# Performance work log

Measured on AMD Instinct MI355X. Metric: run time of the kernel, lower is better.

## Reference

```python
import jax, jax.numpy as jnp
import numpy as np

N = 100000
E = 1600000
F_IN = 128
NHID = 50
NOUT = 50


def gcn_conv(x, W, b, src, dst, n):
    # x: [N, Fin] -> transform first (PyG GCNConv order)
    h = x @ W  # [N, Fout]
    # symmetric normalization with self-loops already included in src/dst
    ones = jnp.ones(src.shape[0], dtype=h.dtype)
    deg = jax.ops.segment_sum(ones, dst, num_segments=n)  # in-degree incl self-loop
    dinv = jnp.where(deg > 0, jax.lax.rsqrt(deg), 0.0)
    norm = dinv[src] * dinv[dst]  # [E']
    msgs = h[src] * norm[:, None]  # gather + scale, [E', Fout]
    out = jax.ops.segment_sum(msgs, dst, num_segments=n)  # scatter-add
    return out + b


def setup_inputs() -> dict:
    key = jax.random.key(0)
    k1, k2, k3, k4, k5, k6 = jax.random.split(key, 6)
    x = jax.random.normal(k1, (N, F_IN), dtype=jnp.float32)
    edge_index = jax.random.randint(k2, (2, E), 0, N, dtype=jnp.int64) if jax.config.read('jax_enable_x64') else jax.random.randint(k2, (2, E), 0, N, dtype=jnp.int32)
    # Glorot-ish init for weights
    W1 = jax.random.normal(k3, (F_IN, NHID), dtype=jnp.float32) * (1.0 / np.sqrt(F_IN))
    b1 = jnp.zeros((NHID,), dtype=jnp.float32)
    W2 = jax.random.normal(k4, (NHID, NOUT), dtype=jnp.float32) * (1.0 / np.sqrt(NHID))
    b2 = jnp.zeros((NOUT,), dtype=jnp.float32)
    return {"x": x, "W1": W1, "b1": b1, "W2": W2, "b2": b2, "edge_index": edge_index}


def reference(x, W1, b1, W2, b2, edge_index):
    n = x.shape[0]
    # add self-loops once (shared by both layers)
    loop = jnp.arange(n, dtype=edge_index.dtype)
    src = jnp.concatenate([edge_index[0], loop])
    dst = jnp.concatenate([edge_index[1], loop])
    h = gcn_conv(x, W1, b1, src, dst, n)
    h = jax.nn.relu(h)
    # dropout is identity in eval mode (training=False)
    out = gcn_conv(h, W2, b2, src, dst, n)
    return out
```

## Files before the change

kernel.cpp:

```cpp
#include <hip/hip_runtime.h>
#include <hip/hip_fp16.h>

#define FIN 128
#define FH 50
#define HSTRIDE 64
#define MAXNB 1024
#define BSHIFT 7
#define BSIZE 128
#define CAP 3072
#define PCHUNK 2048
#define SRCMASK 0x01FFFFFFu

typedef _Float16 f16x8 __attribute__((ext_vector_type(8)));
typedef float f32x4 __attribute__((ext_vector_type(4)));


__global__ __launch_bounds__(256) void partition_kernel(const int* __restrict__ src,
                                                        const int* __restrict__ dst,
                                                        int* __restrict__ gcursor,
                                                        unsigned int* __restrict__ packed,
                                                        int E, int NB) {
    __shared__ int hist[MAXNB];
    __shared__ int wbase[MAXNB];
    int t = threadIdx.x;
    int base = blockIdx.x * PCHUNK;
    for (int i = t; i < NB; i += 256) hist[i] = 0;
    __syncthreads();
#pragma unroll
    for (int i = 0; i < PCHUNK / 256; i++) {
        int e = base + t + i * 256;
        if (e < E) atomicAdd(&hist[dst[e] >> BSHIFT], 1);
    }
    __syncthreads();
    for (int i = t; i < NB; i += 256) {
        int c = hist[i];
        wbase[i] = c ? atomicAdd(&gcursor[i], c) : 0;
        hist[i] = 0;
    }
    __syncthreads();
#pragma unroll
    for (int i = 0; i < PCHUNK / 256; i++) {
        int e = base + t + i * 256;
        if (e < E) {
            unsigned int s = (unsigned int)src[e];
            int d = dst[e];
            int b = d >> BSHIFT;
            int off = atomicAdd(&hist[b], 1);
            packed[(size_t)b * CAP + wbase[b] + off] =
                ((unsigned int)(d & (BSIZE - 1)) << 25) | s;
        }
    }
}

__global__ __launch_bounds__(256) void bucket_build_kernel(const unsigned int* __restrict__ packed,
                                                           const int* __restrict__ gcursor,
                                                           int* __restrict__ rbeg,
                                                           int* __restrict__ rend,
                                                           float* __restrict__ dinv,
                                                           int* __restrict__ csr, int n) {
    __shared__ int degl[BSIZE];
    __shared__ int excl[BSIZE];
    __shared__ int lcur[BSIZE];
    int b = blockIdx.x;
    int t = threadIdx.x;
    int nbeg = b << BSHIFT;
    int sbase = b * CAP;
    int cnt = gcursor[b];
    if (t < BSIZE) degl[t] = 0;
    __syncthreads();
    for (int e = t; e < cnt; e += 256)
        atomicAdd(&degl[packed[sbase + e] >> 25], 1);
    __syncthreads();
    int v = (t < BSIZE) ? degl[t] : 0;
    if (t < BSIZE) excl[t] = v;
    __syncthreads();
    for (int off = 1; off < BSIZE; off <<= 1) {
        int add = (t >= off && t < BSIZE) ? excl[t - off] : 0;
        __syncthreads();
        if (t < BSIZE) excl[t] += add;
        __syncthreads();
    }
    if (t < BSIZE) {
        int ex = excl[t] - v;
        int node = nbeg + t;
        if (node < n) {
            rbeg[node] = sbase + ex;
            rend[node] = sbase + ex + v;
            dinv[node] = rsqrtf((float)v + 1.0f);
        }
        lcur[t] = ex;
    }
    __syncthreads();
    for (int e = t; e < cnt; e += 256) {
        unsigned int w = packed[sbase + e];
        int off = atomicAdd(&lcur[w >> 25], 1);
        csr[sbase + off] = (int)(w & SRCMASK);
    }
}


__global__ __launch_bounds__(256) void wcvt_kernel(const float* __restrict__ W1,
                                                   const float* __restrict__ W2,
                                                   _Float16* __restrict__ WF1,
                                                   _Float16* __restrict__ WF2) {
    int idx = blockIdx.x * 256 + threadIdx.x;
    if (idx < 4 * 4 * 64 * 8) {
        int i = idx & 7, lane = (idx >> 3) & 63, tile = idx >> 9;
        int ct = tile & 3, kt = tile >> 2;
        int k = kt * 32 + ((lane >> 4) << 3) + i;
        int c = ct * 16 + (lane & 15);
        WF1[idx] = (c < FH) ? (_Float16)W1[k * FH + c] : (_Float16)0.f;
    } else if (idx < 8192 + 2 * 4 * 64 * 8) {
        int g = idx - 8192;
        int i = g & 7, lane = (g >> 3) & 63, tile = g >> 9;
        int ct = tile & 3, kt = tile >> 2;
        int k = kt * 32 + ((lane >> 4) << 3) + i;
        int c = ct * 16 + (lane & 15);
        WF2[g] = (k < FH && c < FH) ? (_Float16)W2[k * FH + c] : (_Float16)0.f;
    }
}

__global__ __launch_bounds__(256) void gemm1_kernel(
    const float* __restrict__ x, const _Float16* __restrict__ WF,
    const float* __restrict__ dinv, __half* __restrict__ hs1,
    __half* __restrict__ hs2, int n) {
    int t = threadIdx.x;
    if (blockIdx.x == 0) {
        if (t < HSTRIDE)           hs1[((size_t)n << 6) + t] = __float2half(0.f);
        else if (t < 2 * HSTRIDE)  hs2[((size_t)n << 6) + (t - HSTRIDE)] = __float2half(0.f);
    }
    int tile = blockIdx.x * 4 + (t >> 6);
    int l = t & 63;
    int mt = (n + 15) >> 4;
    if (tile >= mt) return;
    int arow = tile * 16 + (l & 15);
    if (arow >= n) arow = n - 1;
    const f16x8* WB = (const f16x8*)WF;
    f32x4 acc[4] = {{0.f,0.f,0.f,0.f},{0.f,0.f,0.f,0.f},
                    {0.f,0.f,0.f,0.f},{0.f,0.f,0.f,0.f}};
#pragma unroll
    for (int kt = 0; kt < 4; kt++) {
        const float* xp = x + (size_t)arow * FIN + kt * 32 + ((l >> 4) << 3);
        float4 v0 = *(const float4*)xp;
        float4 v1 = *(const float4*)(xp + 4);
        float vs[8] = {v0.x, v0.y, v0.z, v0.w, v1.x, v1.y, v1.z, v1.w};
        f16x8 hi, lo;
#pragma unroll
        for (int i = 0; i < 8; i++) {
            _Float16 h = (_Float16)vs[i];
            hi[i] = h;
            lo[i] = (_Float16)(vs[i] - (float)h);
        }
#pragma unroll
        for (int ct = 0; ct < 4; ct++) {
            f16x8 b = WB[(kt * 4 + ct) * 64 + l];
            acc[ct] = __builtin_amdgcn_mfma_f32_16x16x32_f16(hi, b, acc[ct], 0, 0, 0);
            acc[ct] = __builtin_amdgcn_mfma_f32_16x16x32_f16(lo, b, acc[ct], 0, 0, 0);
        }
    }
    int rbase = tile * 16 + ((l >> 4) << 2);
    float dv[4];
#pragma unroll
    for (int j = 0; j < 4; j++) {
        int r = rbase + j;
        dv[j] = dinv[r < n ? r : 0];
    }
#pragma unroll
    for (int ct = 0; ct < 4; ct++) {
        int col = ct * 16 + (l & 15);
        if (col < FH) {
#pragma unroll
            for (int j = 0; j < 4; j++) {
                int r = rbase + j;
                if (r < n)
                    hs1[((size_t)r << 6) + col] = __float2half(acc[ct][j] * dv[j]);
            }
        }
    }
}

__global__ __launch_bounds__(256) void gemm2_kernel(
    const float* __restrict__ h1, const _Float16* __restrict__ WF,
    const float* __restrict__ dinv, __half* __restrict__ hs2, int n) {
    int t = threadIdx.x;
    int tile = blockIdx.x * 4 + (t >> 6);
    int l = t & 63;
    int mt = (n + 15) >> 4;
    if (tile >= mt) return;
    int arow = tile * 16 + (l & 15);
    if (arow >= n) arow = n - 1;
    const f16x8* WB = (const f16x8*)WF;
    const float* hp = h1 + (size_t)arow * FH;
    f32x4 acc[4] = {{0.f,0.f,0.f,0.f},{0.f,0.f,0.f,0.f},
                    {0.f,0.f,0.f,0.f},{0.f,0.f,0.f,0.f}};
#pragma unroll
    for (int kt = 0; kt < 2; kt++) {
        int k0 = kt * 32 + ((l >> 4) << 3);
        float vs[8];
        if (kt == 0) {
            const float2* p2 = (const float2*)(hp + k0);
#pragma unroll
            for (int q = 0; q < 4; q++) {
                float2 v = p2[q];
                vs[2 * q] = v.x;
                vs[2 * q + 1] = v.y;
            }
        } else {
#pragma unroll
            for (int i = 0; i < 8; i++) {
                int k = k0 + i;
                float v = hp[k < FH ? k : 0];
                vs[i] = (k < FH) ? v : 0.f;
            }
        }
        f16x8 hi, lo;
#pragma unroll
        for (int i = 0; i < 8; i++) {
            _Float16 h = (_Float16)vs[i];
            hi[i] = h;
            lo[i] = (_Float16)(vs[i] - (float)h);
        }
#pragma unroll
        for (int ct = 0; ct < 4; ct++) {
            f16x8 b = WB[(kt * 4 + ct) * 64 + l];
            acc[ct] = __builtin_amdgcn_mfma_f32_16x16x32_f16(hi, b, acc[ct], 0, 0, 0);
            acc[ct] = __builtin_amdgcn_mfma_f32_16x16x32_f16(lo, b, acc[ct], 0, 0, 0);
        }
    }
    int rbase = tile * 16 + ((l >> 4) << 2);
    float dv[4];
#pragma unroll
    for (int j = 0; j < 4; j++) {
        int r = rbase + j;
        dv[j] = dinv[r < n ? r : 0];
    }
#pragma unroll
    for (int ct = 0; ct < 4; ct++) {
        int col = ct * 16 + (l & 15);
        if (col < FH) {
#pragma unroll
            for (int j = 0; j < 4; j++) {
                int r = rbase + j;
                if (r < n)
                    hs2[((size_t)r << 6) + col] = __float2half(acc[ct][j] * dv[j]);
            }
        }
    }
}

__global__ __launch_bounds__(256) void gather_kernel(
    const __half* __restrict__ hs, const int* __restrict__ rbeg,
    const int* __restrict__ rend, const int* __restrict__ csr,
    const float* __restrict__ dinv, const float* __restrict__ b,
    float* __restrict__ out, int n, int do_relu) {
    int wid = blockIdx.x * 4 + (threadIdx.x >> 6);
    int lane = threadIdx.x & 63;
    if (wid >= n) return;
    int sub = lane >> 5;
    int cp  = lane & 31;
    const __half2* h2 = (const __half2*)hs;
    int beg = rbeg[wid];
    int end = rend[wid];
    float2 acc0 = {0.f, 0.f}, acc1 = {0.f, 0.f};
    if (sub == 0) acc0 = __half22float2(h2[(wid << 5) + cp]);
    for (int base = beg; base < end; base += 64) {
        int rem = end - base;
        int idxs = ((lane < rem) ? csr[base + lane] : n) << 5;
        int cnt = rem < 64 ? rem : 64;
        for (int j = 0; j < cnt; j += 16) {
#pragma unroll
            for (int u = 0; u < 8; u += 2) {
                int s0 = __shfl(idxs, j + 2 * u + sub);
                int s1 = __shfl(idxs, j + 2 * (u + 1) + sub);
                float2 f0 = __half22float2(h2[s0 + cp]);
                float2 f1 = __half22float2(h2[s1 + cp]);
                acc0.x += f0.x; acc0.y += f0.y;
                acc1.x += f1.x; acc1.y += f1.y;
            }
        }
    }
    float ax = (acc0.x + acc1.x);
    float ay = (acc0.y + acc1.y);
    ax += __shfl_xor(ax, 32);
    ay += __shfl_xor(ay, 32);
    if (sub == 0 && cp < FH / 2) {
        float dv = dinv[wid];
        const float2* b2 = (const float2*)b;
        float2 bb = b2[cp];
        float ox = fmaf(dv, ax, bb.x);
        float oy = fmaf(dv, ay, bb.y);
        if (do_relu) { ox = fmaxf(ox, 0.f); oy = fmaxf(oy, 0.f); }
        float2* op = (float2*)(out + (size_t)wid * FH);
        op[cp] = make_float2(ox, oy);
    }
}

extern "C" void kernel_launch(void* const* d_in, const int* in_sizes, int n_in,
                              void* d_out, int out_size, void* d_ws, size_t ws_size,
                              hipStream_t stream) {
    const float* x  = (const float*)d_in[0];
    const float* W1 = (const float*)d_in[1];
    const float* b1 = (const float*)d_in[2];
    const float* W2 = (const float*)d_in[3];
    const float* b2 = (const float*)d_in[4];
    const int*   ei = (const int*)d_in[5];

    int n = in_sizes[0] / FIN;
    int E = in_sizes[5] / 2;
    const int* src = ei;
    const int* dst = ei + E;
    int NB = (n + BSIZE - 1) >> BSHIFT;

    char* ws = (char*)d_ws;
    size_t off = 0;
    auto alloc = [&](size_t bytes) {
        void* p = ws + off;
        off = (off + bytes + 511) & ~(size_t)511;
        return p;
    };
    size_t hs_bytes   = (size_t)(n + 1) * HSTRIDE * 2;
    size_t slab_bytes = (size_t)NB * CAP * 4;
    size_t un_bytes   = slab_bytes > hs_bytes ? slab_bytes : hs_bytes;

    int*          gcursor = (int*)alloc((size_t)MAXNB * 4);
    int*          rbeg    = (int*)alloc((size_t)n * 4);
    int*          rend    = (int*)alloc((size_t)n * 4);
    float*        dinv    = (float*)alloc((size_t)n * 4);
    int*          csr     = (int*)alloc(slab_bytes);
    __half*       hs1     = (__half*)alloc(hs_bytes);
    _Float16*     wf1     = (_Float16*)alloc((size_t)8192 * 2);
    _Float16*     wf2     = (_Float16*)alloc((size_t)4096 * 2);
    void*         un      = alloc(un_bytes);
    unsigned int* packed  = (unsigned int*)un;
    __half*       hs2     = (__half*)un;
    float*        out     = (float*)d_out;

    hipMemsetAsync(gcursor, 0, (size_t)MAXNB * 4, stream);

    wcvt_kernel<<<(8192 + 4096 + 255) / 256, 256, 0, stream>>>(W1, W2, wf1, wf2);

    int pChunks = (E + PCHUNK - 1) / PCHUNK;
    partition_kernel<<<pChunks, 256, 0, stream>>>(src, dst, gcursor, packed, E, NB);
    bucket_build_kernel<<<NB, 256, 0, stream>>>(packed, gcursor, rbeg, rend, dinv, csr, n);

    int mt = (n + 15) / 16;
    int gBlocks = (mt + 3) / 4;
    int gatherBlocks = (n + 3) / 4;

    gemm1_kernel<<<gBlocks, 256, 0, stream>>>(x, wf1, dinv, hs1, hs2, n);
    gather_kernel<<<gatherBlocks, 256, 0, stream>>>(hs1, rbeg, rend, csr, dinv, b1, out, n, 1);
    gemm2_kernel<<<gBlocks, 256, 0, stream>>>(out, wf2, dinv, hs2, n);
    gather_kernel<<<gatherBlocks, 256, 0, stream>>>(hs2, rbeg, rend, csr, dinv, b2, out, n, 0);
}
```

Baseline: 251.3 us.

## Replace shared-memory partition histogram with per-edge padded global atomics

```diff
diff --git a/kernel.cpp b/kernel.cpp
--- a/kernel.cpp
+++ b/kernel.cpp
@@ -8,8 +8,9 @@
 #define BSHIFT 7
 #define BSIZE 128
 #define CAP 3072
-#define PCHUNK 2048
+#define EPB 2048
 #define SRCMASK 0x01FFFFFFu
+#define CPAD 16
 
 typedef _Float16 f16x8 __attribute__((ext_vector_type(8)));
 typedef float f32x4 __attribute__((ext_vector_type(4)));
@@ -19,35 +20,30 @@
                                                         const int* __restrict__ dst,
                                                         int* __restrict__ gcursor,
                                                         unsigned int* __restrict__ packed,
-                                                        int E, int NB) {
-    __shared__ int hist[MAXNB];
-    __shared__ int wbase[MAXNB];
-    int t = threadIdx.x;
-    int base = blockIdx.x * PCHUNK;
-    for (int i = t; i < NB; i += 256) hist[i] = 0;
-    __syncthreads();
-#pragma unroll
-    for (int i = 0; i < PCHUNK / 256; i++) {
-        int e = base + t + i * 256;
-        if (e < E) atomicAdd(&hist[dst[e] >> BSHIFT], 1);
-    }
-    __syncthreads();
-    for (int i = t; i < NB; i += 256) {
-        int c = hist[i];
-        wbase[i] = c ? atomicAdd(&gcursor[i], c) : 0;
-        hist[i] = 0;
-    }
-    __syncthreads();
-#pragma unroll
-    for (int i = 0; i < PCHUNK / 256; i++) {
-        int e = base + t + i * 256;
-        if (e < E) {
-            unsigned int s = (unsigned int)src[e];
-            int d = dst[e];
+                                                        int E) {
+    int e0 = (blockIdx.x * 256 + threadIdx.x) * 8;
+    if (e0 >= E) return;
+    if (e0 + 8 <= E) {
+        int4 d0 = *(const int4*)(dst + e0);
+        int4 d1 = *(const int4*)(dst + e0 + 4);
+        int4 s0 = *(const int4*)(src + e0);
+        int4 s1 = *(const int4*)(src + e0 + 4);
+        int ds[8] = {d0.x, d0.y, d0.z, d0.w, d1.x, d1.y, d1.z, d1.w};
+        int ss[8] = {s0.x, s0.y, s0.z, s0.w, s1.x, s1.y, s1.z, s1.w};
+#pragma unroll
+        for (int i = 0; i < 8; i++) {
+            int b = ds[i] >> BSHIFT;
+            int off = atomicAdd(&gcursor[b << 4], 1);
+            packed[(size_t)b * CAP + off] =
+                ((unsigned int)(ds[i] & (BSIZE - 1)) << 25) | (unsigned int)ss[i];
+        }
+    } else {
+        for (int i = 0; i < 8 && e0 + i < E; i++) {
+            int d = dst[e0 + i];
             int b = d >> BSHIFT;
-            int off = atomicAdd(&hist[b], 1);
-            packed[(size_t)b * CAP + wbase[b] + off] =
-                ((unsigned int)(d & (BSIZE - 1)) << 25) | s;
+            int off = atomicAdd(&gcursor[b << 4], 1);
+            packed[(size_t)b * CAP + off] =
+                ((unsigned int)(d & (BSIZE - 1)) << 25) | (unsigned int)src[e0 + i];
         }
     }
 }
@@ -65,11 +61,16 @@
     int t = threadIdx.x;
     int nbeg = b << BSHIFT;
     int sbase = b * CAP;
-    int cnt = gcursor[b];
+    int cnt = gcursor[b << 4];
     if (t < BSIZE) degl[t] = 0;
     __syncthreads();
-    for (int e = t; e < cnt; e += 256)
-        atomicAdd(&degl[packed[sbase + e] >> 25], 1);
+    for (int e4 = t * 4; e4 < cnt; e4 += 1024) {
+        uint4 w = *(const uint4*)(packed + sbase + e4);
+        unsigned int wv[4] = {w.x, w.y, w.z, w.w};
+#pragma unroll
+        for (int i = 0; i < 4; i++)
+            if (e4 + i < cnt) atomicAdd(&degl[wv[i] >> 25], 1);
+    }
     __syncthreads();
     int v = (t < BSIZE) ? degl[t] : 0;
     if (t < BSIZE) excl[t] = v;
@@ -91,10 +92,15 @@
         lcur[t] = ex;
     }
     __syncthreads();
-    for (int e = t; e < cnt; e += 256) {
-        unsigned int w = packed[sbase + e];
-        int off = atomicAdd(&lcur[w >> 25], 1);
-        csr[sbase + off] = (int)(w & SRCMASK);
+    for (int e4 = t * 4; e4 < cnt; e4 += 1024) {
+        uint4 w = *(const uint4*)(packed + sbase + e4);
+        unsigned int wv[4] = {w.x, w.y, w.z, w.w};
+#pragma unroll
+        for (int i = 0; i < 4; i++)
+            if (e4 + i < cnt) {
+                int off = atomicAdd(&lcur[wv[i] >> 25], 1);
+                csr[sbase + off] = (int)(wv[i] & SRCMASK);
+            }
     }
 }
 
@@ -322,7 +328,7 @@
     size_t slab_bytes = (size_t)NB * CAP * 4;
     size_t un_bytes   = slab_bytes > hs_bytes ? slab_bytes : hs_bytes;
 
-    int*          gcursor = (int*)alloc((size_t)MAXNB * 4);
+    int*          gcursor = (int*)alloc((size_t)MAXNB * CPAD * 4);
     int*          rbeg    = (int*)alloc((size_t)n * 4);
     int*          rend    = (int*)alloc((size_t)n * 4);
     float*        dinv    = (float*)alloc((size_t)n * 4);
@@ -335,12 +341,12 @@
     __half*       hs2     = (__half*)un;
     float*        out     = (float*)d_out;
 
-    hipMemsetAsync(gcursor, 0, (size_t)MAXNB * 4, stream);
+    hipMemsetAsync(gcursor, 0, (size_t)MAXNB * CPAD * 4, stream);
 
     wcvt_kernel<<<(8192 + 4096 + 255) / 256, 256, 0, stream>>>(W1, W2, wf1, wf2);
 
-    int pChunks = (E + PCHUNK - 1) / PCHUNK;
-    partition_kernel<<<pChunks, 256, 0, stream>>>(src, dst, gcursor, packed, E, NB);
+    int pBlocks = (E + EPB - 1) / EPB;
+    partition_kernel<<<pBlocks, 256, 0, stream>>>(src, dst, gcursor, packed, E);
     bucket_build_kernel<<<NB, 256, 0, stream>>>(packed, gcursor, rbeg, rend, dinv, csr, n);
 
     int mt = (n + 15) / 16;
```

New measurement: 304.0 us. +20.9%, slower.

## Vectorize partition/bucket loads, pad global cursors, fold memset into weight-convert kernel

Applied to the files above, without the earlier changes.

```diff
diff --git a/kernel.cpp b/kernel.cpp
--- a/kernel.cpp
+++ b/kernel.cpp
@@ -8,8 +8,9 @@
 #define BSHIFT 7
 #define BSIZE 128
 #define CAP 3072
-#define PCHUNK 2048
+#define PCHUNK 3072
 #define SRCMASK 0x01FFFFFFu
+#define CPAD 16
 
 typedef _Float16 f16x8 __attribute__((ext_vector_type(8)));
 typedef float f32x4 __attribute__((ext_vector_type(4)));
@@ -27,27 +28,38 @@
     for (int i = t; i < NB; i += 256) hist[i] = 0;
     __syncthreads();
 #pragma unroll
-    for (int i = 0; i < PCHUNK / 256; i++) {
-        int e = base + t + i * 256;
-        if (e < E) atomicAdd(&hist[dst[e] >> BSHIFT], 1);
+    for (int i = 0; i < PCHUNK / 1024; i++) {
+        int e = base + t * 4 + i * 1024;
+        if (e < E) {
+            int4 d4 = *(const int4*)(dst + e);
+            atomicAdd(&hist[d4.x >> BSHIFT], 1);
+            atomicAdd(&hist[d4.y >> BSHIFT], 1);
+            atomicAdd(&hist[d4.z >> BSHIFT], 1);
+            atomicAdd(&hist[d4.w >> BSHIFT], 1);
+        }
     }
     __syncthreads();
     for (int i = t; i < NB; i += 256) {
         int c = hist[i];
-        wbase[i] = c ? atomicAdd(&gcursor[i], c) : 0;
+        wbase[i] = c ? atomicAdd(&gcursor[i << 4], c) : 0;
         hist[i] = 0;
     }
     __syncthreads();
 #pragma unroll
-    for (int i = 0; i < PCHUNK / 256; i++) {
-        int e = base + t + i * 256;
+    for (int i = 0; i < PCHUNK / 1024; i++) {
+        int e = base + t * 4 + i * 1024;
         if (e < E) {
-            unsigned int s = (unsigned int)src[e];
-            int d = dst[e];
-            int b = d >> BSHIFT;
-            int off = atomicAdd(&hist[b], 1);
-            packed[(size_t)b * CAP + wbase[b] + off] =
-                ((unsigned int)(d & (BSIZE - 1)) << 25) | s;
+            int4 d4 = *(const int4*)(dst + e);
+            int4 s4 = *(const int4*)(src + e);
+            int ds[4] = {d4.x, d4.y, d4.z, d4.w};
+            int ss[4] = {s4.x, s4.y, s4.z, s4.w};
+#pragma unroll
+            for (int j = 0; j < 4; j++) {
+                int b = ds[j] >> BSHIFT;
+                int off = atomicAdd(&hist[b], 1);
+                packed[(size_t)b * CAP + wbase[b] + off] =
+                    ((unsigned int)(ds[j] & (BSIZE - 1)) << 25) | (unsigned int)ss[j];
+            }
         }
     }
 }
@@ -65,11 +77,16 @@
     int t = threadIdx.x;
     int nbeg = b << BSHIFT;
     int sbase = b * CAP;
-    int cnt = gcursor[b];
+    int cnt = gcursor[b << 4];
     if (t < BSIZE) degl[t] = 0;
     __syncthreads();
-    for (int e = t; e < cnt; e += 256)
-        atomicAdd(&degl[packed[sbase + e] >> 25], 1);
+    for (int e4 = t * 4; e4 < cnt; e4 += 1024) {
+        uint4 w = *(const uint4*)(packed + sbase + e4);
+        unsigned int wv[4] = {w.x, w.y, w.z, w.w};
+#pragma unroll
+        for (int i = 0; i < 4; i++)
+            if (e4 + i < cnt) atomicAdd(&degl[wv[i] >> 25], 1);
+    }
     __syncthreads();
     int v = (t < BSIZE) ? degl[t] : 0;
     if (t < BSIZE) excl[t] = v;
@@ -91,10 +108,15 @@
         lcur[t] = ex;
     }
     __syncthreads();
-    for (int e = t; e < cnt; e += 256) {
-        unsigned int w = packed[sbase + e];
-        int off = atomicAdd(&lcur[w >> 25], 1);
-        csr[sbase + off] = (int)(w & SRCMASK);
+    for (int e4 = t * 4; e4 < cnt; e4 += 1024) {
+        uint4 w = *(const uint4*)(packed + sbase + e4);
+        unsigned int wv[4] = {w.x, w.y, w.z, w.w};
+#pragma unroll
+        for (int i = 0; i < 4; i++)
+            if (e4 + i < cnt) {
+                int off = atomicAdd(&lcur[wv[i] >> 25], 1);
+                csr[sbase + off] = (int)(wv[i] & SRCMASK);
+            }
     }
 }
 
@@ -102,8 +124,10 @@
 __global__ __launch_bounds__(256) void wcvt_kernel(const float* __restrict__ W1,
                                                    const float* __restrict__ W2,
                                                    _Float16* __restrict__ WF1,
-                                                   _Float16* __restrict__ WF2) {
+                                                   _Float16* __restrict__ WF2,
+                                                   int* __restrict__ gcursor) {
     int idx = blockIdx.x * 256 + threadIdx.x;
+    if (idx < MAXNB * CPAD) gcursor[idx] = 0;
     if (idx < 4 * 4 * 64 * 8) {
         int i = idx & 7, lane = (idx >> 3) & 63, tile = idx >> 9;
         int ct = tile & 3, kt = tile >> 2;
@@ -322,7 +346,7 @@
     size_t slab_bytes = (size_t)NB * CAP * 4;
     size_t un_bytes   = slab_bytes > hs_bytes ? slab_bytes : hs_bytes;
 
-    int*          gcursor = (int*)alloc((size_t)MAXNB * 4);
+    int*          gcursor = (int*)alloc((size_t)MAXNB * CPAD * 4);
     int*          rbeg    = (int*)alloc((size_t)n * 4);
     int*          rend    = (int*)alloc((size_t)n * 4);
     float*        dinv    = (float*)alloc((size_t)n * 4);
@@ -335,12 +359,10 @@
     __half*       hs2     = (__half*)un;
     float*        out     = (float*)d_out;
 
-    hipMemsetAsync(gcursor, 0, (size_t)MAXNB * 4, stream);
-
-    wcvt_kernel<<<(8192 + 4096 + 255) / 256, 256, 0, stream>>>(W1, W2, wf1, wf2);
-
-    int pChunks = (E + PCHUNK - 1) / PCHUNK;
-    partition_kernel<<<pChunks, 256, 0, stream>>>(src, dst, gcursor, packed, E, NB);
+    wcvt_kernel<<<64, 256, 0, stream>>>(W1, W2, wf1, wf2, gcursor);
+
+    int pBlocks = (E + PCHUNK - 1) / PCHUNK;
+    partition_kernel<<<pBlocks, 256, 0, stream>>>(src, dst, gcursor, packed, E, NB);
     bucket_build_kernel<<<NB, 256, 0, stream>>>(packed, gcursor, rbeg, rend, dinv, csr, n);
 
     int mt = (n + 15) / 16;
```

Result: no change. 253.4 us (+0.8%).
